# Performance work log

Measured on AMD Instinct MI355X. Metric: run time of the kernel, lower is better.

The kernel has to match this reference:

```python
import jax, jax.numpy as jnp
import numpy as np

# Dims matching init_kwargs: k=5, inplanes=512, planes=512, m=4, padding=None, stride=1
N, C, H, W = 32, 512, 56, 56
M = 4
CM = C // M          # 128, = group count (depthwise)
K1 = 5               # dynamic kernel size
K2 = 3               # atrous kernel size (dilation 2)
P2 = 512 // 2        # planes // 2


def setup_inputs() -> dict:
    key = jax.random.key(0)
    ks = jax.random.split(key, 13)
    s = lambda i, shape: jax.random.normal(ks[i], shape, jnp.float32) * 0.05
    return dict(
        x=jax.random.normal(ks[0], (N, C, H, W), jnp.float32),
        W_conv=s(1, (CM, C)), b_conv=s(2, (CM,)),        # self.conv (1x1)
        wk=s(3, (K1 * K1,)), bk=s(4, (K1 * K1,)),        # self.conv_kernel (1->k*k, 1x1)
        wck=s(5, ()), bck=s(6, ()),                      # self.conv_k (1->1, 1x1 scalar affine)
        wk2=s(7, (K2 * K2,)), bk2=s(8, (K2 * K2,)),      # self.conv_kernel2 (1->9)
        wck2=s(9, ()), bck2=s(10, ()),                   # self.conv_k2
        W_fuse=s(11, (P2, CM)), b_fuse=s(12, (P2,)),     # self.fuse (1x1)
    )


def _dw_conv(f, kern, dil, pad):
    # Per-sample depthwise conv: fold batch into groups -> single conv call.
    # f: [N, CM, H, W], kern: [N, CM, k, k]
    n, cm, h, w = f.shape
    fr = f.reshape(1, n * cm, h, w)
    kr = kern.reshape(n * cm, 1, kern.shape[-2], kern.shape[-1])
    o = jax.lax.conv_general_dilated(
        fr, kr, window_strides=(1, 1), padding=[(pad, pad), (pad, pad)],
        rhs_dilation=(dil, dil), feature_group_count=n * cm,
        dimension_numbers=('NCHW', 'OIHW', 'NCHW'))
    return o.reshape(n, cm, h, w)


def reference(x, W_conv, b_conv, wk, bk, wck, bck, wk2, bk2, wck2, bck2, W_fuse, b_fuse):
    # f = relu(conv(x));  g = relu(conv(avg_pool(x)))
    f = jax.nn.relu(jnp.einsum('nchw,oc->nohw', x, W_conv) + b_conv[None, :, None, None])
    g = jax.nn.relu(x.mean((2, 3)) @ W_conv.T + b_conv)  # [N, CM]
    # dynamic per-channel kernels: (g*wk + bk)*wck + bck, reshaped to [N, CM, k, k]
    kern1 = ((g[:, :, None] * wk + bk) * wck + bck).reshape(N, CM, K1, K1)
    kern2 = ((g[:, :, None] * wk2 + bk2) * wck2 + bck2).reshape(N, CM, K2, K2)
    o1 = _dw_conv(f, kern1, dil=1, pad=(K1 - 1) // 2)   # plain branch
    o2 = _dw_conv(f, kern2, dil=2, pad=2)               # atrous branch
    y1 = jnp.einsum('nchw,oc->nohw', o1, W_fuse) + b_fuse[None, :, None, None]
    y2 = jnp.einsum('nchw,oc->nohw', o2, W_fuse) + b_fuse[None, :, None, None]
    return jnp.concatenate([y1, y2], axis=1)  # [N, planes, H, W]
```

## Files before the change

### kernel.cpp

```cpp
#include <hip/hip_runtime.h>

typedef unsigned short u16;
typedef unsigned int   u32;

#define NB   32
#define CIN  512
#define CM   128
#define P2   256
#define HW   3136
#define HD   56

typedef __attribute__((ext_vector_type(8))) short           short8;
typedef __attribute__((ext_vector_type(8))) unsigned short  ushort8;
typedef __attribute__((ext_vector_type(4))) unsigned short  ushort4_t;
typedef __attribute__((ext_vector_type(4))) float           f32x4;
typedef __attribute__((ext_vector_type(2))) unsigned int    u32x2;

__device__ __forceinline__ float b2f(u16 u) {
    union { u32 i; float f; } v; v.i = ((u32)u) << 16; return v.f;
}
__device__ __forceinline__ u16 f2b(float f) {
    u32 u = __builtin_bit_cast(u32, f);
    u32 r = (u + 0x7fffu + ((u >> 16) & 1u)) >> 16;
    return (u16)r;
}

__global__ __launch_bounds__(256) void init_kernel(const float* __restrict__ Wc,
                                                   const float* __restrict__ Wf,
                                                   u16* __restrict__ Wcb,
                                                   u16* __restrict__ Wfb,
                                                   float* __restrict__ ym) {
    int i = blockIdx.x * 256 + threadIdx.x;
    if (i < CM * CIN) { Wcb[i] = f2b(Wc[i]); return; }
    i -= CM * CIN;
    if (i < P2 * CM) { Wfb[i] = f2b(Wf[i]); return; }
    i -= P2 * CM;
    if (i < NB * CM) ym[i] = 0.f;
}

__global__ __launch_bounds__(256) void gemm1_kernel(
    const float* __restrict__ In,
    const u16* __restrict__ Wm, const float* __restrict__ bias,
    u16* __restrict__ Out, float* __restrict__ ym)
{
    __shared__ u16 ldsT[128 * 40];

    const int n    = blockIdx.z;
    const int hw0  = blockIdx.x * 128;
    const int tid  = threadIdx.x;
    const int wave = tid >> 6, lane = tid & 63;
    const int wm   = (wave >> 1) * 64;
    const int wn   = (wave & 1) * 64;
    const int qa   = lane >> 4;
    const int l15  = lane & 15;

    f32x4 acc[4][4] = {};

    const int kpair = tid >> 4;
    const int c0    = (tid & 15) * 8;
    const int hwc   = hw0 + c0;
    const bool cok  = (hwc < HW);

    for (int k0 = 0; k0 < CIN; k0 += 32) {
        __syncthreads();
        u32 pk[8];
        {
            f32x4 a0 = {0,0,0,0}, a1 = {0,0,0,0}, d0 = {0,0,0,0}, d1 = {0,0,0,0};
            if (cok) {
                const float* p0 = In + (size_t)n * CIN * HW
                                + (size_t)(k0 + kpair * 2) * HW + hwc;
                a0 = *(const f32x4*)p0;
                a1 = *(const f32x4*)(p0 + 4);
                d0 = *(const f32x4*)(p0 + HW);
                d1 = *(const f32x4*)(p0 + HW + 4);
            }
            float fa[8] = {a0[0],a0[1],a0[2],a0[3],a1[0],a1[1],a1[2],a1[3]};
            float fb[8] = {d0[0],d0[1],d0[2],d0[3],d1[0],d1[1],d1[2],d1[3]};
            #pragma unroll
            for (int e = 0; e < 8; ++e) {
                u32 ua = __builtin_bit_cast(u32, fa[e]) + 0x8000u;
                u32 ub = __builtin_bit_cast(u32, fb[e]) + 0x8000u;
                pk[e] = __builtin_amdgcn_perm(ub, ua, 0x07060302u);
            }
        }
        #pragma unroll
        for (int e = 0; e < 8; ++e)
            *(u32*)&ldsT[(c0 + e) * 40 + kpair * 2] = pk[e];
        __syncthreads();

        short8 b[4];
        #pragma unroll
        for (int nt = 0; nt < 4; ++nt) {
            int row = wm + nt * 16 + l15;
            b[nt] = *(const short8*)(Wm + (size_t)row * CIN + k0 + qa * 8);
        }
        #pragma unroll
        for (int ht = 0; ht < 4; ++ht) {
            short8 a = *(const short8*)&ldsT[(wn + ht * 16 + l15) * 40 + qa * 8];
            #pragma unroll
            for (int nt = 0; nt < 4; ++nt)
                acc[ht][nt] = __builtin_amdgcn_mfma_f32_16x16x32_bf16(a, b[nt], acc[ht][nt], 0, 0, 0);
        }
    }

    #pragma unroll
    for (int nt = 0; nt < 4; ++nt) {
        const int m = wm + nt * 16 + l15;
        const float bv = bias[m];
        float s = 0.f;
        #pragma unroll
        for (int ht = 0; ht < 4; ++ht) {
            f32x4 v = acc[ht][nt];
            s += v[0] + v[1] + v[2] + v[3];
            int hwb = hw0 + wn + ht * 16;
            if (hwb < HW) {
                float v0 = fmaxf(v[0] + bv, 0.f);
                float v1 = fmaxf(v[1] + bv, 0.f);
                float v2 = fmaxf(v[2] + bv, 0.f);
                float v3 = fmaxf(v[3] + bv, 0.f);
                u32x2 pkv;
                pkv.x = (u32)f2b(v0) | ((u32)f2b(v1) << 16);
                pkv.y = (u32)f2b(v2) | ((u32)f2b(v3) << 16);
                *(u32x2*)(Out + ((size_t)n * CM + m) * HW + hwb + qa * 4) = pkv;
            }
        }
        s += __shfl_xor(s, 16);
        s += __shfl_xor(s, 32);
        if (lane < 16) atomicAdd(&ym[n * CM + m], s);
    }
}

#define PD 60
__global__ __launch_bounds__(256) void dw_kernel(
    const u16* __restrict__ f, const float* __restrict__ ym,
    const float* __restrict__ bc,
    const float* __restrict__ wk,  const float* __restrict__ bk,
    const float* __restrict__ wck, const float* __restrict__ bck,
    const float* __restrict__ wk2, const float* __restrict__ bk2,
    const float* __restrict__ wck2,const float* __restrict__ bck2,
    u16* __restrict__ o1, u16* __restrict__ o2)
{
    const int ncm = blockIdx.x;
    __shared__ float fpl[PD * PD];
    __shared__ float kc1[25], kc2[9];

    {
        int t = threadIdx.x;
        if (t < 120) { fpl[t] = 0.f; fpl[58 * PD + t] = 0.f; }
        else if (t < 232) {
            int u = t - 120;
            int r = 2 + (u >> 1), c = u & 1;
            fpl[r * PD + c]      = 0.f;
            fpl[r * PD + 58 + c] = 0.f;
        }
    }
    const float gv = fmaxf(ym[ncm] * (1.0f / HW) + bc[ncm & (CM - 1)], 0.f);
    if (threadIdx.x < 25) {
        int t = threadIdx.x;
        kc1[t] = (gv * wk[t] + bk[t]) * wck[0] + bck[0];
    } else if (threadIdx.x >= 32 && threadIdx.x < 41) {
        int t = threadIdx.x - 32;
        kc2[t] = (gv * wk2[t] + bk2[t]) * wck2[0] + bck2[0];
    }
    __syncthreads();

    const size_t base = (size_t)ncm * HW;
    const u32x2* fp = (const u32x2*)(f + base);
    for (int i = threadIdx.x; i < HW / 4; i += 256) {
        u32x2 v = fp[i];
        int px = 4 * i;
        int h = px / HD, w = px - h * HD;
        float* dst = &fpl[(h + 2) * PD + (w + 2)];
        dst[0] = b2f((u16)v.x);
        dst[1] = b2f((u16)(v.x >> 16));
        dst[2] = b2f((u16)v.y);
        dst[3] = b2f((u16)(v.y >> 16));
    }
    __syncthreads();

    u32* o1p = (u32*)(o1 + base);
    u32* o2p = (u32*)(o2 + base);
    for (int u = threadIdx.x; u < 392; u += 256) {
        int h  = u / 7;
        int gq = u - h * 7;
        int w0 = gq * 8;
        float a1[8] = {}, a2[8] = {};
        #pragma unroll
        for (int di = 0; di < 5; ++di) {
            const float* row = &fpl[(h + di) * PD + w0];
            float r[12];
            #pragma unroll
            for (int x = 0; x < 12; ++x) r[x] = row[x];
            #pragma unroll
            for (int j = 0; j < 5; ++j) {
                float kv = kc1[di * 5 + j];
                #pragma unroll
                for (int e = 0; e < 8; ++e) a1[e] = fmaf(kv, r[j + e], a1[e]);
            }
            if ((di & 1) == 0) {
                int i2 = di >> 1;
                #pragma unroll
                for (int j = 0; j < 3; ++j) {
                    float kv = kc2[i2 * 3 + j];
                    #pragma unroll
                    for (int e = 0; e < 8; ++e) a2[e] = fmaf(kv, r[2 * j + e], a2[e]);
                }
            }
        }
        int ob = (h * HD + w0) >> 1;
        #pragma unroll
        for (int e = 0; e < 4; ++e) {
            o1p[ob + e] = (u32)f2b(a1[2 * e]) | ((u32)f2b(a1[2 * e + 1]) << 16);
            o2p[ob + e] = (u32)f2b(a2[2 * e]) | ((u32)f2b(a2[2 * e + 1]) << 16);
        }
    }
}

#define FSTR 140
__global__ __launch_bounds__(256) void fuse_kernel(
    const u16* __restrict__ o1, const u16* __restrict__ o2,
    const u16* __restrict__ Wfb, const float* __restrict__ bias,
    float* __restrict__ out)
{
    __shared__ u16 ldsT[64 * FSTR];

    const int n   = blockIdx.z;
    const int br  = blockIdx.y;
    const u16* In = br ? o2 : o1;
    const int ch_off = br ? P2 : 0;
    const int hw0 = blockIdx.x * 64;
    const int tid = threadIdx.x;
    const int wave = tid >> 6, lane = tid & 63;
    const int wm  = wave * 64;
    const int qa  = lane >> 4, l15 = lane & 15;

    {
        const int c0 = (tid & 7) * 8;
        const int kp = tid >> 3;
        #pragma unroll
        for (int kk = 0; kk < CM; kk += 64) {
            const u16* p0 = In + (size_t)n * CM * HW + (size_t)(kk + 2 * kp) * HW + hw0 + c0;
            ushort8 v0 = *(const ushort8*)p0;
            ushort8 v1 = *(const ushort8*)(p0 + HW);
            #pragma unroll
            for (int e = 0; e < 8; ++e)
                *(u32*)&ldsT[(c0 + e) * FSTR + kk + 2 * kp] = (u32)v0[e] | ((u32)v1[e] << 16);
        }
    }
    __syncthreads();

    f32x4 acc[4][4] = {};
    #pragma unroll
    for (int q = 0; q < 4; ++q) {
        short8 b[4];
        #pragma unroll
        for (int nt = 0; nt < 4; ++nt) {
            int row = wm + nt * 16 + l15;
            b[nt] = *(const short8*)(Wfb + (size_t)row * CM + q * 32 + qa * 8);
        }
        #pragma unroll
        for (int ht = 0; ht < 4; ++ht) {
            int c = ht * 16 + l15;
            union { ushort4_t h[2]; short8 v; } au;
            au.h[0] = *(const ushort4_t*)&ldsT[c * FSTR + q * 32 + qa * 8];
            au.h[1] = *(const ushort4_t*)&ldsT[c * FSTR + q * 32 + qa * 8 + 4];
            #pragma unroll
            for (int nt = 0; nt < 4; ++nt)
                acc[ht][nt] = __builtin_amdgcn_mfma_f32_16x16x32_bf16(au.v, b[nt], acc[ht][nt], 0, 0, 0);
        }
    }

    #pragma unroll
    for (int nt = 0; nt < 4; ++nt) {
        const int m = wm + nt * 16 + l15;
        const float bv = bias[m];
        float* orow = out + ((size_t)n * 512 + ch_off + m) * HW + hw0 + qa * 4;
        #pragma unroll
        for (int ht = 0; ht < 4; ++ht) {
            f32x4 v;
            v[0] = acc[ht][nt][0] + bv;
            v[1] = acc[ht][nt][1] + bv;
            v[2] = acc[ht][nt][2] + bv;
            v[3] = acc[ht][nt][3] + bv;
            *(f32x4*)(orow + ht * 16) = v;
        }
    }
}

extern "C" void kernel_launch(void* const* d_in, const int* in_sizes, int n_in,
                              void* d_out, int out_size, void* d_ws, size_t ws_size,
                              hipStream_t stream) {
    const float* x     = (const float*)d_in[0];
    const float* Wconv = (const float*)d_in[1];
    const float* bconv = (const float*)d_in[2];
    const float* wk    = (const float*)d_in[3];
    const float* bk    = (const float*)d_in[4];
    const float* wck   = (const float*)d_in[5];
    const float* bck   = (const float*)d_in[6];
    const float* wk2   = (const float*)d_in[7];
    const float* bk2   = (const float*)d_in[8];
    const float* wck2  = (const float*)d_in[9];
    const float* bck2  = (const float*)d_in[10];
    const float* Wfuse = (const float*)d_in[11];
    const float* bfuse = (const float*)d_in[12];
    float* out = (float*)d_out;

    float* ym  = (float*)d_ws;
    u16*   Wcb = (u16*)(ym + NB * CM);
    u16*   Wfb = Wcb + CM * CIN;
    u16*   f   = Wfb + P2 * CM;
    u16*   o1  = f  + (size_t)NB * CM * HW;
    u16*   o2  = o1 + (size_t)NB * CM * HW;

    {
        int tot = CM * CIN + P2 * CM + NB * CM;
        init_kernel<<<dim3((tot + 255) / 256), 256, 0, stream>>>(Wconv, Wfuse, Wcb, Wfb, ym);
    }
    gemm1_kernel<<<dim3(25, 1, NB), 256, 0, stream>>>(x, Wcb, bconv, f, ym);
    dw_kernel<<<dim3(NB * CM), 256, 0, stream>>>(f, ym, bconv, wk, bk, wck, bck,
                                                 wk2, bk2, wck2, bck2, o1, o2);
    fuse_kernel<<<dim3(49, 2, NB), 256, 0, stream>>>(o1, o2, Wfb, bfuse, out);
}
```

Before: 457.8 us.

## Double-buffer gemm1 LDS with prefetch, smaller tiles, and XOR-swizzled LDS layouts

The first 1x1 GEMM now uses 64-column tiles (49x32 blocks) with a K step of 64. It double-buffers the transposed bf16 input in LDS and prefetches the next K slice from global memory while MFMAs run on the current one, which leaves one barrier per iteration. Both gemm1 and the fuse kernel switch to an XOR-swizzled LDS layout, so the fuse kernel does one 16-byte LDS read per operand instead of two 8-byte reads. The aim is to hide global load latency, raise occupancy and cut LDS bank conflicts. The cost is more LDS per block and more blocks that each reuse the weights less.

Result: faster. 447.0 us (-2.4%).

```diff
diff --git a/kernel.cpp b/kernel.cpp
--- a/kernel.cpp
+++ b/kernel.cpp
@@ -12,7 +12,6 @@
 
 typedef __attribute__((ext_vector_type(8))) short           short8;
 typedef __attribute__((ext_vector_type(8))) unsigned short  ushort8;
-typedef __attribute__((ext_vector_type(4))) unsigned short  ushort4_t;
 typedef __attribute__((ext_vector_type(4))) float           f32x4;
 typedef __attribute__((ext_vector_type(2))) unsigned int    u32x2;
 
@@ -38,69 +37,95 @@
     if (i < NB * CM) ym[i] = 0.f;
 }
 
+#define G1S 72
 __global__ __launch_bounds__(256) void gemm1_kernel(
     const float* __restrict__ In,
     const u16* __restrict__ Wm, const float* __restrict__ bias,
     u16* __restrict__ Out, float* __restrict__ ym)
 {
-    __shared__ u16 ldsT[128 * 40];
-
-    const int n    = blockIdx.z;
-    const int hw0  = blockIdx.x * 128;
+    __shared__ u16 lds[2 * 64 * G1S];
+
+    const int n    = blockIdx.y;
+    const int hw0  = blockIdx.x * 64;
     const int tid  = threadIdx.x;
     const int wave = tid >> 6, lane = tid & 63;
     const int wm   = (wave >> 1) * 64;
-    const int wn   = (wave & 1) * 64;
+    const int wn   = (wave & 1) * 32;
     const int qa   = lane >> 4;
     const int l15  = lane & 15;
 
-    f32x4 acc[4][4] = {};
-
-    const int kpair = tid >> 4;
-    const int c0    = (tid & 15) * 8;
-    const int hwc   = hw0 + c0;
-    const bool cok  = (hwc < HW);
-
-    for (int k0 = 0; k0 < CIN; k0 += 32) {
-        __syncthreads();
-        u32 pk[8];
-        {
-            f32x4 a0 = {0,0,0,0}, a1 = {0,0,0,0}, d0 = {0,0,0,0}, d1 = {0,0,0,0};
-            if (cok) {
-                const float* p0 = In + (size_t)n * CIN * HW
-                                + (size_t)(k0 + kpair * 2) * HW + hwc;
-                a0 = *(const f32x4*)p0;
-                a1 = *(const f32x4*)(p0 + 4);
-                d0 = *(const f32x4*)(p0 + HW);
-                d1 = *(const f32x4*)(p0 + HW + 4);
+    f32x4 acc[2][4] = {};
+
+    const int kp   = tid >> 3;
+    const int c0   = (tid & 7) * 8;
+    const int sw   = tid & 7;
+    const int wbase = c0 * G1S + (((kp >> 2) ^ sw) << 3) + 2 * (kp & 3);
+    const float* inb = In + (size_t)n * CIN * HW + hw0 + c0;
+
+    {
+        const float* p = inb + (size_t)(2 * kp) * HW;
+        f32x4 a0 = *(const f32x4*)p;
+        f32x4 a1 = *(const f32x4*)(p + 4);
+        f32x4 d0 = *(const f32x4*)(p + HW);
+        f32x4 d1 = *(const f32x4*)(p + HW + 4);
+        float fa[8] = {a0[0],a0[1],a0[2],a0[3],a1[0],a1[1],a1[2],a1[3]};
+        float fb[8] = {d0[0],d0[1],d0[2],d0[3],d1[0],d1[1],d1[2],d1[3]};
+        #pragma unroll
+        for (int e = 0; e < 8; ++e) {
+            u32 ua = __builtin_bit_cast(u32, fa[e]) + 0x8000u;
+            u32 ub = __builtin_bit_cast(u32, fb[e]) + 0x8000u;
+            *(u32*)&lds[wbase + e * G1S] = __builtin_amdgcn_perm(ub, ua, 0x07060302u);
+        }
+    }
+    __syncthreads();
+
+    for (int k0 = 0; k0 < CIN; k0 += 64) {
+        u16* cbuf = &lds[((k0 >> 6) & 1) * (64 * G1S)];
+        u16* nbuf = &lds[(~(k0 >> 6) & 1) * (64 * G1S)];
+        const bool more = (k0 + 64 < CIN);
+
+        f32x4 a0, a1, d0, d1;
+        if (more) {
+            const float* p = inb + (size_t)(k0 + 64 + 2 * kp) * HW;
+            a0 = *(const f32x4*)p;
+            a1 = *(const f32x4*)(p + 4);
+            d0 = *(const f32x4*)(p + HW);
+            d1 = *(const f32x4*)(p + HW + 4);
+        }
+
+        short8 b0[4], b1[4];
+        #pragma unroll
+        for (int nt = 0; nt < 4; ++nt) {
+            const u16* wr = Wm + (size_t)(wm + nt * 16 + l15) * CIN + k0 + qa * 8;
+            b0[nt] = *(const short8*)wr;
+            b1[nt] = *(const short8*)(wr + 32);
+        }
+
+        #pragma unroll
+        for (int ht = 0; ht < 2; ++ht) {
+            const int col = wn + ht * 16 + l15;
+            const int csz = (col >> 3) & 7;
+            const u16* cb = cbuf + col * G1S;
+            short8 x0 = *(const short8*)(cb + ((qa ^ csz) << 3));
+            short8 x1 = *(const short8*)(cb + (((qa + 4) ^ csz) << 3));
+            #pragma unroll
+            for (int nt = 0; nt < 4; ++nt) {
+                acc[ht][nt] = __builtin_amdgcn_mfma_f32_16x16x32_bf16(x0, b0[nt], acc[ht][nt], 0, 0, 0);
+                acc[ht][nt] = __builtin_amdgcn_mfma_f32_16x16x32_bf16(x1, b1[nt], acc[ht][nt], 0, 0, 0);
             }
+        }
+
+        if (more) {
             float fa[8] = {a0[0],a0[1],a0[2],a0[3],a1[0],a1[1],a1[2],a1[3]};
             float fb[8] = {d0[0],d0[1],d0[2],d0[3],d1[0],d1[1],d1[2],d1[3]};
             #pragma unroll
             for (int e = 0; e < 8; ++e) {
                 u32 ua = __builtin_bit_cast(u32, fa[e]) + 0x8000u;
                 u32 ub = __builtin_bit_cast(u32, fb[e]) + 0x8000u;
-                pk[e] = __builtin_amdgcn_perm(ub, ua, 0x07060302u);
+                *(u32*)&nbuf[wbase + e * G1S] = __builtin_amdgcn_perm(ub, ua, 0x07060302u);
             }
         }
-        #pragma unroll
-        for (int e = 0; e < 8; ++e)
-            *(u32*)&ldsT[(c0 + e) * 40 + kpair * 2] = pk[e];
         __syncthreads();
-
-        short8 b[4];
-        #pragma unroll
-        for (int nt = 0; nt < 4; ++nt) {
-            int row = wm + nt * 16 + l15;
-            b[nt] = *(const short8*)(Wm + (size_t)row * CIN + k0 + qa * 8);
-        }
-        #pragma unroll
-        for (int ht = 0; ht < 4; ++ht) {
-            short8 a = *(const short8*)&ldsT[(wn + ht * 16 + l15) * 40 + qa * 8];
-            #pragma unroll
-            for (int nt = 0; nt < 4; ++nt)
-                acc[ht][nt] = __builtin_amdgcn_mfma_f32_16x16x32_bf16(a, b[nt], acc[ht][nt], 0, 0, 0);
-        }
     }
 
     #pragma unroll
@@ -109,20 +134,18 @@
         const float bv = bias[m];
         float s = 0.f;
         #pragma unroll
-        for (int ht = 0; ht < 4; ++ht) {
+        for (int ht = 0; ht < 2; ++ht) {
             f32x4 v = acc[ht][nt];
             s += v[0] + v[1] + v[2] + v[3];
-            int hwb = hw0 + wn + ht * 16;
-            if (hwb < HW) {
-                float v0 = fmaxf(v[0] + bv, 0.f);
-                float v1 = fmaxf(v[1] + bv, 0.f);
-                float v2 = fmaxf(v[2] + bv, 0.f);
-                float v3 = fmaxf(v[3] + bv, 0.f);
-                u32x2 pkv;
-                pkv.x = (u32)f2b(v0) | ((u32)f2b(v1) << 16);
-                pkv.y = (u32)f2b(v2) | ((u32)f2b(v3) << 16);
-                *(u32x2*)(Out + ((size_t)n * CM + m) * HW + hwb + qa * 4) = pkv;
-            }
+            const int hwb = hw0 + wn + ht * 16;
+            float v0 = fmaxf(v[0] + bv, 0.f);
+            float v1 = fmaxf(v[1] + bv, 0.f);
+            float v2 = fmaxf(v[2] + bv, 0.f);
+            float v3 = fmaxf(v[3] + bv, 0.f);
+            u32x2 pkv;
+            pkv.x = (u32)f2b(v0) | ((u32)f2b(v1) << 16);
+            pkv.y = (u32)f2b(v2) | ((u32)f2b(v3) << 16);
+            *(u32x2*)(Out + ((size_t)n * CM + m) * HW + hwb + qa * 4) = pkv;
         }
         s += __shfl_xor(s, 16);
         s += __shfl_xor(s, 32);
@@ -216,7 +239,7 @@
     }
 }
 
-#define FSTR 140
+#define FSTR 144
 __global__ __launch_bounds__(256) void fuse_kernel(
     const u16* __restrict__ o1, const u16* __restrict__ o2,
     const u16* __restrict__ Wfb, const float* __restrict__ bias,
@@ -237,14 +260,16 @@
     {
         const int c0 = (tid & 7) * 8;
         const int kp = tid >> 3;
+        const int sw = tid & 7;
         #pragma unroll
         for (int kk = 0; kk < CM; kk += 64) {
             const u16* p0 = In + (size_t)n * CM * HW + (size_t)(kk + 2 * kp) * HW + hw0 + c0;
             ushort8 v0 = *(const ushort8*)p0;
             ushort8 v1 = *(const ushort8*)(p0 + HW);
+            const int wb = c0 * FSTR + ((((kk >> 3) + (kp >> 2)) ^ sw) << 3) + 2 * (kp & 3);
             #pragma unroll
             for (int e = 0; e < 8; ++e)
-                *(u32*)&ldsT[(c0 + e) * FSTR + kk + 2 * kp] = (u32)v0[e] | ((u32)v1[e] << 16);
+                *(u32*)&ldsT[wb + e * FSTR] = (u32)v0[e] | ((u32)v1[e] << 16);
         }
     }
     __syncthreads();
@@ -260,13 +285,12 @@
         }
         #pragma unroll
         for (int ht = 0; ht < 4; ++ht) {
-            int c = ht * 16 + l15;
-            union { ushort4_t h[2]; short8 v; } au;
-            au.h[0] = *(const ushort4_t*)&ldsT[c * FSTR + q * 32 + qa * 8];
-            au.h[1] = *(const ushort4_t*)&ldsT[c * FSTR + q * 32 + qa * 8 + 4];
+            const int col = ht * 16 + l15;
+            const int csz = (col >> 3) & 7;
+            short8 av = *(const short8*)&ldsT[col * FSTR + (((q * 4 + qa) ^ csz) << 3)];
             #pragma unroll
             for (int nt = 0; nt < 4; ++nt)
-                acc[ht][nt] = __builtin_amdgcn_mfma_f32_16x16x32_bf16(au.v, b[nt], acc[ht][nt], 0, 0, 0);
+                acc[ht][nt] = __builtin_amdgcn_mfma_f32_16x16x32_bf16(av, b[nt], acc[ht][nt], 0, 0, 0);
         }
     }
 
@@ -316,7 +340,7 @@
         int tot = CM * CIN + P2 * CM + NB * CM;
         init_kernel<<<dim3((tot + 255) / 256), 256, 0, stream>>>(Wconv, Wfuse, Wcb, Wfb, ym);
     }
-    gemm1_kernel<<<dim3(25, 1, NB), 256, 0, stream>>>(x, Wcb, bconv, f, ym);
+    gemm1_kernel<<<dim3(49, NB), 256, 0, stream>>>(x, Wcb, bconv, f, ym);
     dw_kernel<<<dim3(NB * CM), 256, 0, stream>>>(f, ym, bconv, wk, bk, wck, bck,
                                                  wk2, bk2, wck2, bck2, o1, o2);
     fuse_kernel<<<dim3(49, 2, NB), 256, 0, stream>>>(o1, o2, Wfb, bfuse, out);
```
